# Kernel optimization log

Measured on AMD Instinct MI355X. Metric: run time of the kernel, lower is better.

## Reference

```python
import jax, jax.numpy as jnp
import numpy as np

IN_DIM, K, D, ITERS, EPS = 512, 8, 128, 3, 1e-8
LN_EPS = 1e-5

def _ln(x, g, b):
    m = jnp.mean(x, axis=-1, keepdims=True)
    v = jnp.var(x, axis=-1, keepdims=True)
    return (x - m) * jax.lax.rsqrt(v + LN_EPS) * g + b

def setup_inputs() -> dict:
    key = jax.random.key(0)
    ks = jax.random.split(key, 16)
    B, C, H, W = 64, IN_DIM, 32, 32
    s = lambda fan: 1.0 / np.sqrt(fan)
    inp = {
        'x': jax.random.normal(ks[0], (B, C, H, W), jnp.float32),
        'noise': jax.random.normal(ks[1], (B, K, D), jnp.float32),
        'slot_mu': jax.random.normal(ks[2], (1, K, D), jnp.float32) * 0.02,
        'slot_log_sigma': jnp.zeros((1, K, D), jnp.float32),
        'Wp': jax.random.uniform(ks[3], (IN_DIM, D), jnp.float32, -s(IN_DIM), s(IN_DIM)),
        'bp': jnp.zeros((D,), jnp.float32),
        'g_in': jnp.ones((D,), jnp.float32), 'b_in': jnp.zeros((D,), jnp.float32),
        'Wq': jax.random.uniform(ks[4], (D, D), jnp.float32, -s(D), s(D)),
        'bq': jnp.zeros((D,), jnp.float32),
        'Wk': jax.random.uniform(ks[5], (D, D), jnp.float32, -s(D), s(D)),
        'bk': jnp.zeros((D,), jnp.float32),
        'Wv': jax.random.uniform(ks[6], (D, D), jnp.float32, -s(D), s(D)),
        'bv': jnp.zeros((D,), jnp.float32),
        'W_ih': jax.random.uniform(ks[7], (3 * D, D), jnp.float32, -s(D), s(D)),
        'W_hh': jax.random.uniform(ks[8], (3 * D, D), jnp.float32, -s(D), s(D)),
        'b_ih': jax.random.uniform(ks[9], (3 * D,), jnp.float32, -s(D), s(D)),
        'b_hh': jax.random.uniform(ks[10], (3 * D,), jnp.float32, -s(D), s(D)),
        'W1': jax.random.uniform(ks[11], (D, 2 * D), jnp.float32, -s(D), s(D)),
        'b1': jnp.zeros((2 * D,), jnp.float32),
        'W2': jax.random.uniform(ks[12], (2 * D, D), jnp.float32, -s(2 * D), s(2 * D)),
        'b2': jnp.zeros((D,), jnp.float32),
        'g_slots': jnp.ones((D,), jnp.float32), 'b_slots': jnp.zeros((D,), jnp.float32),
        'g_mlp': jnp.ones((D,), jnp.float32), 'b_mlp': jnp.zeros((D,), jnp.float32),
    }
    return inp

def reference(x, noise, slot_mu, slot_log_sigma, Wp, bp, g_in, b_in,
              Wq, bq, Wk, bk, Wv, bv, W_ih, W_hh, b_ih, b_hh,
              W1, b1, W2, b2, g_slots, b_slots, g_mlp, b_mlp):
    B, C, H, W = x.shape
    N = H * W
    scale = D ** -0.5
    x_flat = x.reshape(B, C, N).transpose(0, 2, 1)          # [B,N,C]
    inputs = _ln(x_flat @ Wp + bp, g_in, b_in)              # [B,N,D]
    slots = slot_mu + jnp.exp(slot_log_sigma) * noise       # [B,K,D]
    k = inputs @ Wk + bk                                    # k/v are loop-invariant
    v = inputs @ Wv + bv
    attn = None
    for _ in range(ITERS):
        slots_prev = slots
        q = _ln(slots, g_slots, b_slots) @ Wq + bq          # [B,K,D]
        logits = jnp.einsum('bkd,bnd->bkn', q, k) * scale
        attn = jax.nn.softmax(logits, axis=1)               # softmax over slots
        attn_norm = attn / (jnp.sum(attn, axis=-1, keepdims=True) + EPS)
        updates = jnp.einsum('bkn,bnd->bkd', attn_norm, v)  # [B,K,D]
        # GRUCell (PyTorch gate order r,z,n)
        u2 = updates.reshape(B * K, D)
        h = slots_prev.reshape(B * K, D)
        gx = u2 @ W_ih.T + b_ih
        gh = h @ W_hh.T + b_hh
        xr, xz, xn = jnp.split(gx, 3, axis=-1)
        hr, hz, hn = jnp.split(gh, 3, axis=-1)
        r = jax.nn.sigmoid(xr + hr)
        z = jax.nn.sigmoid(xz + hz)
        n = jnp.tanh(xn + r * hn)
        slots = ((1.0 - z) * n + z * h).reshape(B, K, D)
        hmid = jax.nn.gelu(_ln(slots, g_mlp, b_mlp) @ W1 + b1, approximate=False)
        slots = slots + hmid @ W2 + b2
    return slots, attn
```

## Files before the change

### kernel.cpp

```cpp
#include <hip/hip_runtime.h>
#include <hip/hip_bf16.h>
#include <math.h>

#define B_ 64
#define C_ 512
#define N_ 1024
#define D_ 128
#define K_ 8

typedef __attribute__((ext_vector_type(8))) short bf16x8;
typedef __attribute__((ext_vector_type(4))) float f32x4;
typedef unsigned short ushort_t;

__device__ __forceinline__ unsigned short f2bs(float f) {
    union { __hip_bfloat16 h; unsigned short s; } u;
    u.h = __float2bfloat16(f);
    return u.s;
}
__device__ __forceinline__ float bs2f(unsigned short s) {
    union { unsigned int u; float f; } v;
    v.u = ((unsigned int)s) << 16;
    return v.f;
}
__device__ __forceinline__ float sigmoidf_(float x) { return 1.0f / (1.0f + expf(-x)); }
__device__ __forceinline__ float gelu_exact(float x) {
    return 0.5f * x * (1.0f + erff(x * 0.7071067811865476f));
}

__global__ __launch_bounds__(256) void prep_weights(
    const float* __restrict__ Wp, const float* __restrict__ Wk,
    const float* __restrict__ Wv, const float* __restrict__ W_ih,
    const float* __restrict__ W_hh,
    ushort_t* __restrict__ WpT, ushort_t* __restrict__ WkT,
    ushort_t* __restrict__ WvT, float* __restrict__ WTih,
    float* __restrict__ WThh)
{
    int tid = blockIdx.x * 256 + threadIdx.x;
    {
        int c = tid >> 7, d = tid & 127;
        WpT[d * 512 + c] = f2bs(Wp[tid]);
    }
    if (tid < 16384) {
        int c = tid >> 7, d = tid & 127;
        WkT[d * 128 + c] = f2bs(Wk[tid]);
        WvT[d * 128 + c] = f2bs(Wv[tid]);
    }
    if (tid < 49152) {
        int j = tid >> 7, c = tid & 127;
        WTih[c * 384 + j] = W_ih[tid];
        WThh[c * 384 + j] = W_hh[tid];
    }
}

__global__ __launch_bounds__(256) void proj_ln_mfma(
    const float* __restrict__ x, const ushort_t* __restrict__ WpT,
    const float* __restrict__ bp, const float* __restrict__ g_in,
    const float* __restrict__ b_in, ushort_t* __restrict__ outb)
{
    __shared__ ushort_t Al[64 * 40];
    __shared__ ushort_t Bl[128 * 40];
    __shared__ float red[64][2][2];
    const int t = threadIdx.x;
    const int b = blockIdx.x >> 4;
    const int n0 = (blockIdx.x & 15) << 6;
    const int w = t >> 6, lane = t & 63;
    const int quad = lane >> 4, m = lane & 15;
    const int rowoff = (w >> 1) << 5;
    const int coloff = (w & 1) << 6;

    f32x4 acc[2][4];
#pragma unroll
    for (int r = 0; r < 2; ++r)
#pragma unroll
        for (int c = 0; c < 4; ++c) acc[r][c] = (f32x4){0.f, 0.f, 0.f, 0.f};

    const float* xb = x + (size_t)b * (C_ * N_);
    for (int c0 = 0; c0 < C_; c0 += 32) {
#pragma unroll
        for (int i = 0; i < 8; ++i) {
            int idx = t + (i << 8);
            int cc = idx >> 6, nn = idx & 63;
            Al[nn * 40 + cc] = f2bs(xb[(size_t)(c0 + cc) * N_ + n0 + nn]);
        }
#pragma unroll
        for (int i = 0; i < 2; ++i) {
            int idx = t + (i << 8);
            int d = idx >> 2, seg = idx & 3;
            *(bf16x8*)&Bl[d * 40 + seg * 8] =
                *(const bf16x8*)&WpT[d * 512 + c0 + seg * 8];
        }
        __syncthreads();
        bf16x8 af[2], bfr[4];
#pragma unroll
        for (int r = 0; r < 2; ++r)
            af[r] = *(const bf16x8*)&Al[(rowoff + 16 * r + m) * 40 + quad * 8];
#pragma unroll
        for (int c = 0; c < 4; ++c)
            bfr[c] = *(const bf16x8*)&Bl[(coloff + 16 * c + m) * 40 + quad * 8];
#pragma unroll
        for (int r = 0; r < 2; ++r)
#pragma unroll
            for (int c = 0; c < 4; ++c)
                acc[r][c] = __builtin_amdgcn_mfma_f32_16x16x32_bf16(af[r], bfr[c], acc[r][c], 0, 0, 0);
        __syncthreads();
    }
    float gv[4], bv[4], bpv[4];
#pragma unroll
    for (int c = 0; c < 4; ++c) {
        int col = coloff + 16 * c + m;
        bpv[c] = bp[col]; gv[c] = g_in[col]; bv[c] = b_in[col];
    }
#pragma unroll
    for (int r = 0; r < 2; ++r)
#pragma unroll
        for (int c = 0; c < 4; ++c)
#pragma unroll
            for (int g = 0; g < 4; ++g) acc[r][c][g] += bpv[c];

#pragma unroll
    for (int r = 0; r < 2; ++r) {
#pragma unroll
        for (int g = 0; g < 4; ++g) {
            float s = 0.f, s2 = 0.f;
#pragma unroll
            for (int c = 0; c < 4; ++c) { float v = acc[r][c][g]; s += v; s2 += v * v; }
#pragma unroll
            for (int off = 1; off < 16; off <<= 1) {
                s += __shfl_xor(s, off, 64);
                s2 += __shfl_xor(s2, off, 64);
            }
            if (m == 0) {
                int row = rowoff + 16 * r + quad * 4 + g;
                red[row][w & 1][0] = s;
                red[row][w & 1][1] = s2;
            }
        }
    }
    __syncthreads();
#pragma unroll
    for (int r = 0; r < 2; ++r) {
#pragma unroll
        for (int g = 0; g < 4; ++g) {
            int row = rowoff + 16 * r + quad * 4 + g;
            float s = red[row][0][0] + red[row][1][0];
            float s2 = red[row][0][1] + red[row][1][1];
            float mean = s * (1.f / 128.f);
            float var = s2 * (1.f / 128.f) - mean * mean;
            float rs = rsqrtf(var + 1e-5f);
            size_t base = ((size_t)b * N_ + n0 + row) * D_;
#pragma unroll
            for (int c = 0; c < 4; ++c) {
                int col = coloff + 16 * c + m;
                float v = (acc[r][c][g] - mean) * rs * gv[c] + bv[c];
                outb[base + col] = f2bs(v);
            }
        }
    }
}

__global__ __launch_bounds__(256) void kv_mfma(
    const ushort_t* __restrict__ A,
    const ushort_t* __restrict__ WkT, const float* __restrict__ bk,
    const ushort_t* __restrict__ WvT, const float* __restrict__ bv,
    ushort_t* __restrict__ kout, ushort_t* __restrict__ vout)
{
    __shared__ ushort_t Al[64 * 40];
    __shared__ ushort_t Bk[128 * 40];
    __shared__ ushort_t Bv[128 * 40];
    const int t = threadIdx.x;
    const int row0 = blockIdx.x << 6;
    const int w = t >> 6, lane = t & 63;
    const int quad = lane >> 4, m = lane & 15;
    const int is_v = w >> 1;
    const int rowoff = (w & 1) << 5;

    f32x4 acc[2][8];
#pragma unroll
    for (int r = 0; r < 2; ++r)
#pragma unroll
        for (int c = 0; c < 8; ++c) acc[r][c] = (f32x4){0.f, 0.f, 0.f, 0.f};

    for (int c0 = 0; c0 < D_; c0 += 32) {
#pragma unroll
        for (int i = 0; i < 2; ++i) {
            int idx = t + (i << 8);
            int rr = idx >> 3, cc4 = (idx & 7) << 2;
            *(ushort4*)&Al[rr * 40 + cc4] =
                *(const ushort4*)&A[(size_t)(row0 + rr) * D_ + c0 + cc4];
        }
#pragma unroll
        for (int i = 0; i < 2; ++i) {
            int idx = t + (i << 8);
            int d = idx >> 2, seg = idx & 3;
            *(bf16x8*)&Bk[d * 40 + seg * 8] =
                *(const bf16x8*)&WkT[d * 128 + c0 + seg * 8];
            *(bf16x8*)&Bv[d * 40 + seg * 8] =
                *(const bf16x8*)&WvT[d * 128 + c0 + seg * 8];
        }
        __syncthreads();
        const ushort_t* Bsrc = is_v ? Bv : Bk;
        bf16x8 af[2], bfr[8];
#pragma unroll
        for (int r = 0; r < 2; ++r)
            af[r] = *(const bf16x8*)&Al[(rowoff + 16 * r + m) * 40 + quad * 8];
#pragma unroll
        for (int c = 0; c < 8; ++c)
            bfr[c] = *(const bf16x8*)&Bsrc[(16 * c + m) * 40 + quad * 8];
#pragma unroll
        for (int r = 0; r < 2; ++r)
#pragma unroll
            for (int c = 0; c < 8; ++c)
                acc[r][c] = __builtin_amdgcn_mfma_f32_16x16x32_bf16(af[r], bfr[c], acc[r][c], 0, 0, 0);
        __syncthreads();
    }
    const float* bias = is_v ? bv : bk;
    ushort_t* dst = is_v ? vout : kout;
    float bval[8];
#pragma unroll
    for (int c = 0; c < 8; ++c) bval[c] = bias[16 * c + m];
#pragma unroll
    for (int r = 0; r < 2; ++r) {
#pragma unroll
        for (int g = 0; g < 4; ++g) {
            int row = rowoff + 16 * r + quad * 4 + g;
            size_t base = (size_t)(row0 + row) * D_;
#pragma unroll
            for (int c = 0; c < 8; ++c)
                dst[base + 16 * c + m] = f2bs(acc[r][c][g] + bval[c]);
        }
    }
}

__global__ __launch_bounds__(256) void slots_init_kernel(
    const float* __restrict__ noise, const float* __restrict__ mu,
    const float* __restrict__ lsig, float* __restrict__ slots)
{
    int idx = blockIdx.x * 256 + threadIdx.x;
    int kd = idx & (K_ * D_ - 1);
    slots[idx] = mu[kd] + expf(lsig[kd]) * noise[idx];
}

__global__ __launch_bounds__(128) void q_ln_kernel(
    const float* __restrict__ slots, const float* __restrict__ g_slots,
    const float* __restrict__ b_slots, const float* __restrict__ Wq,
    const float* __restrict__ bq, float* __restrict__ qbuf,
    float* __restrict__ upd, float* __restrict__ S)
{
    __shared__ float sl[128], sl2[128];
    __shared__ float mrs[2];
    const int t = threadIdx.x;
    const int row = blockIdx.x;
    sl[t] = slots[(size_t)row * D_ + t];
    upd[(size_t)row * D_ + t] = 0.0f;
    if (t == 0) S[row] = 0.0f;
    __syncthreads();
    if (t < 64) {
        float v0 = sl[t], v1 = sl[t + 64];
        float s = v0 + v1, s2 = v0 * v0 + v1 * v1;
        for (int off = 32; off > 0; off >>= 1) {
            s += __shfl_down(s, off, 64);
            s2 += __shfl_down(s2, off, 64);
        }
        if (t == 0) {
            float mean = s * (1.f / 128.f);
            float var = s2 * (1.f / 128.f) - mean * mean;
            mrs[0] = mean; mrs[1] = rsqrtf(var + 1e-5f);
        }
    }
    __syncthreads();
    sl2[t] = (sl[t] - mrs[0]) * mrs[1] * g_slots[t] + b_slots[t];
    __syncthreads();
    float a = bq[t];
    for (int c = 0; c < 128; ++c) a = fmaf(sl2[c], Wq[(size_t)c * D_ + t], a);
    qbuf[(size_t)row * D_ + t] = a;
}

__global__ __launch_bounds__(256) void attn_kernel(
    const ushort_t* __restrict__ kb, const float* __restrict__ qbuf,
    float* __restrict__ attn, float* __restrict__ S,
    float* __restrict__ attn_out, int write_attn)
{
    __shared__ float qs[8][128];
    __shared__ float kt[64][129];
    __shared__ float lg[8][66];
    const int t = threadIdx.x;
    const int n0 = blockIdx.x << 6;
    const int b = blockIdx.y;
    const float SCALE = 0.08838834764831845f;

#pragma unroll
    for (int i = 0; i < 4; ++i) {
        int idx = t + (i << 8);
        int k = idx >> 7, d = idx & 127;
        qs[k][d] = qbuf[((size_t)b * K_ + k) * D_ + d];
    }
#pragma unroll
    for (int i = 0; i < 8; ++i) {
        int idx = t + (i << 8);
        int rr = idx >> 5, d4 = (idx & 31) << 2;
        ushort4 kv4 = *(const ushort4*)&kb[((size_t)b * N_ + n0 + rr) * D_ + d4];
        kt[rr][d4] = bs2f(kv4.x); kt[rr][d4 + 1] = bs2f(kv4.y);
        kt[rr][d4 + 2] = bs2f(kv4.z); kt[rr][d4 + 3] = bs2f(kv4.w);
    }
    __syncthreads();
    {
        int nn = t & 63, kg = t >> 6;
        float a0 = 0.f, a1 = 0.f;
        for (int d = 0; d < 128; ++d) {
            float kv = kt[nn][d];
            a0 = fmaf(qs[kg][d], kv, a0);
            a1 = fmaf(qs[kg + 4][d], kv, a1);
        }
        lg[kg][nn] = a0 * SCALE;
        lg[kg + 4][nn] = a1 * SCALE;
    }
    __syncthreads();
    if (t < 64) {
        float mx = lg[0][t];
#pragma unroll
        for (int k = 1; k < 8; ++k) mx = fmaxf(mx, lg[k][t]);
        float e[8]; float s = 0.f;
#pragma unroll
        for (int k = 0; k < 8; ++k) { e[k] = expf(lg[k][t] - mx); s += e[k]; }
        float inv = 1.0f / s;
#pragma unroll
        for (int k = 0; k < 8; ++k) lg[k][t] = e[k] * inv;
#pragma unroll
        for (int k = 0; k < 8; ++k) {
            float pv = e[k] * inv;
            for (int off = 32; off > 0; off >>= 1) pv += __shfl_down(pv, off, 64);
            if (t == 0) atomicAdd(&S[b * K_ + k], pv);
        }
    }
    __syncthreads();
    {
        int nn = t & 63, kg = t >> 6;
        float p0 = lg[kg][nn], p1 = lg[kg + 4][nn];
        size_t i0 = ((size_t)b * K_ + kg) * N_ + n0 + nn;
        size_t i1 = ((size_t)b * K_ + kg + 4) * N_ + n0 + nn;
        attn[i0] = p0;
        attn[i1] = p1;
        if (write_attn) { attn_out[i0] = p0; attn_out[i1] = p1; }
    }
}

__global__ __launch_bounds__(256) void updates_kernel(
    const float* __restrict__ attn, const ushort_t* __restrict__ vb,
    float* __restrict__ upd)
{
    __shared__ float vt[64][129];
    __shared__ float at[8][66];
    const int t = threadIdx.x;
    const int b = blockIdx.y;
    const int nbase = blockIdx.x << 8;
    const int d = t & 127, kk = t >> 7;
    float a0 = 0.f, a1 = 0.f, a2 = 0.f, a3 = 0.f;
    for (int st = 0; st < 4; ++st) {
        int n0 = nbase + (st << 6);
#pragma unroll
        for (int i = 0; i < 8; ++i) {
            int idx = t + (i << 8);
            int rr = idx >> 5, d4 = (idx & 31) << 2;
            ushort4 v4 = *(const ushort4*)&vb[((size_t)b * N_ + n0 + rr) * D_ + d4];
            vt[rr][d4] = bs2f(v4.x); vt[rr][d4 + 1] = bs2f(v4.y);
            vt[rr][d4 + 2] = bs2f(v4.z); vt[rr][d4 + 3] = bs2f(v4.w);
        }
#pragma unroll
        for (int i = 0; i < 2; ++i) {
            int idx = t + (i << 8);
            int k = idx >> 6, nn = idx & 63;
            at[k][nn] = attn[((size_t)b * K_ + k) * N_ + n0 + nn];
        }
        __syncthreads();
        for (int nn = 0; nn < 64; ++nn) {
            float vv = vt[nn][d];
            a0 = fmaf(at[kk][nn], vv, a0);
            a1 = fmaf(at[kk + 2][nn], vv, a1);
            a2 = fmaf(at[kk + 4][nn], vv, a2);
            a3 = fmaf(at[kk + 6][nn], vv, a3);
        }
        __syncthreads();
    }
    atomicAdd(&upd[((size_t)b * K_ + kk) * D_ + d], a0);
    atomicAdd(&upd[((size_t)b * K_ + kk + 2) * D_ + d], a1);
    atomicAdd(&upd[((size_t)b * K_ + kk + 4) * D_ + d], a2);
    atomicAdd(&upd[((size_t)b * K_ + kk + 6) * D_ + d], a3);
}

__global__ __launch_bounds__(256) void gru_mlp_kernel(
    const float* __restrict__ upd, const float* __restrict__ S,
    float* __restrict__ slots,
    const float* __restrict__ WTih, const float* __restrict__ WThh,
    const float* __restrict__ b_ih, const float* __restrict__ b_hh,
    const float* __restrict__ W1, const float* __restrict__ b1,
    const float* __restrict__ W2, const float* __restrict__ b2,
    const float* __restrict__ g_mlp, const float* __restrict__ b_mlp,
    float* __restrict__ out_slots, int final_iter)
{
    __shared__ float u[128], h[128], gx[384], gh[384], sn[128], tt[128], hm[256];
    __shared__ float mrs[2];
    const int t = threadIdx.x;
    const int row = blockIdx.x;
    if (t < 128) {
        float inv = 1.0f / (S[row] + 1e-8f);
        u[t] = upd[(size_t)row * D_ + t] * inv;
        h[t] = slots[(size_t)row * D_ + t];
    }
    __syncthreads();
    {
        int j = t;
        float ax = 0.f, ah = 0.f;
        for (int c = 0; c < 128; ++c) {
            float uc = u[c], hc = h[c];
            ax = fmaf(uc, WTih[(size_t)c * 384 + j], ax);
            ah = fmaf(hc, WThh[(size_t)c * 384 + j], ah);
        }
        gx[j] = ax + b_ih[j];
        gh[j] = ah + b_hh[j];
    }
    if (t < 128) {
        int j = 256 + t;
        float ax = 0.f, ah = 0.f;
        for (int c = 0; c < 128; ++c) {
            float uc = u[c], hc = h[c];
            ax = fmaf(uc, WTih[(size_t)c * 384 + j], ax);
            ah = fmaf(hc, WThh[(size_t)c * 384 + j], ah);
        }
        gx[j] = ax + b_ih[j];
        gh[j] = ah + b_hh[j];
    }
    __syncthreads();
    if (t < 128) {
        float r = sigmoidf_(gx[t] + gh[t]);
        float z = sigmoidf_(gx[t + 128] + gh[t + 128]);
        float nv = tanhf(gx[t + 256] + r * gh[t + 256]);
        sn[t] = (1.0f - z) * nv + z * h[t];
    }
    __syncthreads();
    if (t < 64) {
        float v0 = sn[t], v1 = sn[t + 64];
        float s = v0 + v1, s2 = v0 * v0 + v1 * v1;
        for (int off = 32; off > 0; off >>= 1) {
            s += __shfl_down(s, off, 64);
            s2 += __shfl_down(s2, off, 64);
        }
        if (t == 0) {
            float mean = s * (1.f / 128.f);
            float var = s2 * (1.f / 128.f) - mean * mean;
            mrs[0] = mean; mrs[1] = rsqrtf(var + 1e-5f);
        }
    }
    __syncthreads();
    if (t < 128) tt[t] = (sn[t] - mrs[0]) * mrs[1] * g_mlp[t] + b_mlp[t];
    __syncthreads();
    {
        float a = 0.f;
        for (int c = 0; c < 128; ++c) a = fmaf(tt[c], W1[(size_t)c * 256 + t], a);
        hm[t] = gelu_exact(a + b1[t]);
    }
    __syncthreads();
    if (t < 128) {
        float a = sn[t] + b2[t];
        for (int j = 0; j < 256; ++j) a = fmaf(hm[j], W2[(size_t)j * D_ + t], a);
        slots[(size_t)row * D_ + t] = a;
        if (final_iter) out_slots[(size_t)row * D_ + t] = a;
    }
}

extern "C" void kernel_launch(void* const* d_in, const int* in_sizes, int n_in,
                              void* d_out, int out_size, void* d_ws, size_t ws_size,
                              hipStream_t stream) {
    const float* x       = (const float*)d_in[0];
    const float* noise   = (const float*)d_in[1];
    const float* slot_mu = (const float*)d_in[2];
    const float* slot_ls = (const float*)d_in[3];
    const float* Wp      = (const float*)d_in[4];
    const float* bp      = (const float*)d_in[5];
    const float* g_in    = (const float*)d_in[6];
    const float* b_in    = (const float*)d_in[7];
    const float* Wq      = (const float*)d_in[8];
    const float* bq      = (const float*)d_in[9];
    const float* Wk      = (const float*)d_in[10];
    const float* bk      = (const float*)d_in[11];
    const float* Wv      = (const float*)d_in[12];
    const float* bv      = (const float*)d_in[13];
    const float* W_ih    = (const float*)d_in[14];
    const float* W_hh    = (const float*)d_in[15];
    const float* b_ih    = (const float*)d_in[16];
    const float* b_hh    = (const float*)d_in[17];
    const float* W1      = (const float*)d_in[18];
    const float* b1      = (const float*)d_in[19];
    const float* W2      = (const float*)d_in[20];
    const float* b2      = (const float*)d_in[21];
    const float* g_slots = (const float*)d_in[22];
    const float* b_slots = (const float*)d_in[23];
    const float* g_mlp   = (const float*)d_in[24];
    const float* b_mlp   = (const float*)d_in[25];

    float* out_slots = (float*)d_out;
    float* out_attn  = (float*)d_out + 65536;

    float* wsf = (float*)d_ws;
    ushort_t* inputsb = (ushort_t*)wsf;
    ushort_t* kb = (ushort_t*)(wsf + 4194304);
    ushort_t* vb = (ushort_t*)(wsf + 8388608);
    float* slots = wsf + 12582912;
    float* qbuf  = wsf + 12648448;
    float* attn  = wsf + 12713984;
    float* upd   = wsf + 13238272;
    float* S     = wsf + 13303808;
    ushort_t* WpT = (ushort_t*)(wsf + 13304320);
    ushort_t* WkT = (ushort_t*)(wsf + 13337088);
    ushort_t* WvT = (ushort_t*)(wsf + 13345280);
    float* WTih = wsf + 13353472;
    float* WThh = wsf + 13402624;

    prep_weights<<<dim3(256), dim3(256), 0, stream>>>(
        Wp, Wk, Wv, W_ih, W_hh, WpT, WkT, WvT, WTih, WThh);
    proj_ln_mfma<<<dim3(1024), dim3(256), 0, stream>>>(x, WpT, bp, g_in, b_in, inputsb);
    kv_mfma<<<dim3(1024), dim3(256), 0, stream>>>(inputsb, WkT, bk, WvT, bv, kb, vb);
    slots_init_kernel<<<dim3(256), dim3(256), 0, stream>>>(noise, slot_mu, slot_ls, slots);

    for (int it = 0; it < 3; ++it) {
        int last = (it == 2) ? 1 : 0;
        q_ln_kernel<<<dim3(512), dim3(128), 0, stream>>>(
            slots, g_slots, b_slots, Wq, bq, qbuf, upd, S);
        attn_kernel<<<dim3(16, 64), dim3(256), 0, stream>>>(
            kb, qbuf, attn, S, out_attn, last);
        updates_kernel<<<dim3(4, 64), dim3(256), 0, stream>>>(attn, vb, upd);
        gru_mlp_kernel<<<dim3(512), dim3(256), 0, stream>>>(
            upd, S, slots, WTih, WThh, b_ih, b_hh, W1, b1, W2, b2, g_mlp, b_mlp,
            out_slots, last);
    }
}
```

Before: 447.8 us.

## Fuse attention logits, softmax and PV into one kernel; fold q-proj into GRU

Merges the attention-logit/softmax kernel and the updates kernel into a single attn_pv kernel per (batch, quarter of N). The attention probabilities stay in shared memory instead of round-tripping through global memory, and per-block partial sums replace atomics. The slot LayerNorm plus Q projection moves into the tail of the GRU/MLP kernel, and slot init is fused with the first Q computation, cutting kernel launches per iteration from four to two. In exchange the fused kernel uses large shared memory with only 256 blocks of 512 threads, which may limit occupancy, and it adds a small reduction over the partial buffers.

Result: faster. 407.9 us (-8.9%).

```diff
diff --git a/kernel.cpp b/kernel.cpp
--- a/kernel.cpp
+++ b/kernel.cpp
@@ -231,28 +231,22 @@
     }
 }
 
-__global__ __launch_bounds__(256) void slots_init_kernel(
+__global__ __launch_bounds__(128) void init_q(
     const float* __restrict__ noise, const float* __restrict__ mu,
-    const float* __restrict__ lsig, float* __restrict__ slots)
-{
-    int idx = blockIdx.x * 256 + threadIdx.x;
-    int kd = idx & (K_ * D_ - 1);
-    slots[idx] = mu[kd] + expf(lsig[kd]) * noise[idx];
-}
-
-__global__ __launch_bounds__(128) void q_ln_kernel(
-    const float* __restrict__ slots, const float* __restrict__ g_slots,
-    const float* __restrict__ b_slots, const float* __restrict__ Wq,
-    const float* __restrict__ bq, float* __restrict__ qbuf,
-    float* __restrict__ upd, float* __restrict__ S)
+    const float* __restrict__ lsig,
+    const float* __restrict__ g_slots, const float* __restrict__ b_slots,
+    const float* __restrict__ Wq, const float* __restrict__ bq,
+    float* __restrict__ slots, float* __restrict__ qbuf)
 {
     __shared__ float sl[128], sl2[128];
     __shared__ float mrs[2];
     const int t = threadIdx.x;
     const int row = blockIdx.x;
-    sl[t] = slots[(size_t)row * D_ + t];
-    upd[(size_t)row * D_ + t] = 0.0f;
-    if (t == 0) S[row] = 0.0f;
+    const int b = row >> 3;
+    const int kd = (row & 7) * 128 + t;
+    float sv = mu[kd] + expf(lsig[kd]) * noise[b * 1024 + kd];
+    slots[(size_t)row * D_ + t] = sv;
+    sl[t] = sv;
     __syncthreads();
     if (t < 64) {
         float v0 = sl[t], v1 = sl[t + 64];
@@ -275,135 +269,183 @@
     qbuf[(size_t)row * D_ + t] = a;
 }
 
-__global__ __launch_bounds__(256) void attn_kernel(
-    const ushort_t* __restrict__ kb, const float* __restrict__ qbuf,
-    float* __restrict__ attn, float* __restrict__ S,
-    float* __restrict__ attn_out, int write_attn)
+__global__ __launch_bounds__(512, 2) void attn_pv(
+    const ushort_t* __restrict__ kb, const ushort_t* __restrict__ vb,
+    const float* __restrict__ qbuf,
+    float* __restrict__ S_part, float* __restrict__ upd_part,
+    float* __restrict__ out_attn, int last)
 {
-    __shared__ float qs[8][128];
-    __shared__ float kt[64][129];
-    __shared__ float lg[8][66];
+    __shared__ __align__(16) char scratch[69632];
+    __shared__ __align__(16) float at8[8][264];
+    __shared__ __align__(16) float qs[8][132];
+    __shared__ float red2[4][8];
+    ushort_t* kvt = (ushort_t*)scratch;
+    float* red = (float*)scratch;
+
     const int t = threadIdx.x;
-    const int n0 = blockIdx.x << 6;
-    const int b = blockIdx.y;
+    const int qd = blockIdx.x, b = blockIdx.y;
+    const int nbase = qd << 8;
+    const int wv = t >> 6, lane = t & 63;
     const float SCALE = 0.08838834764831845f;
 
-#pragma unroll
-    for (int i = 0; i < 4; ++i) {
-        int idx = t + (i << 8);
-        int k = idx >> 7, d = idx & 127;
-        qs[k][d] = qbuf[((size_t)b * K_ + k) * D_ + d];
-    }
+    for (int i = t; i < 1024; i += 512)
+        qs[i >> 7][i & 127] = qbuf[(size_t)b * 1024 + i];
 #pragma unroll
     for (int i = 0; i < 8; ++i) {
-        int idx = t + (i << 8);
-        int rr = idx >> 5, d4 = (idx & 31) << 2;
-        ushort4 kv4 = *(const ushort4*)&kb[((size_t)b * N_ + n0 + rr) * D_ + d4];
-        kt[rr][d4] = bs2f(kv4.x); kt[rr][d4 + 1] = bs2f(kv4.y);
-        kt[rr][d4 + 2] = bs2f(kv4.z); kt[rr][d4 + 3] = bs2f(kv4.w);
-    }
-    __syncthreads();
+        int idx = t + (i << 9);
+        int rr = idx >> 4, u8 = (idx & 15) << 3;
+        *(bf16x8*)&kvt[rr * 136 + u8] =
+            *(const bf16x8*)&kb[((size_t)b * N_ + nbase + rr) * D_ + u8];
+    }
+    __syncthreads();
+
     {
-        int nn = t & 63, kg = t >> 6;
-        float a0 = 0.f, a1 = 0.f;
-        for (int d = 0; d < 128; ++d) {
-            float kv = kt[nn][d];
-            a0 = fmaf(qs[kg][d], kv, a0);
-            a1 = fmaf(qs[kg + 4][d], kv, a1);
-        }
-        lg[kg][nn] = a0 * SCALE;
-        lg[kg + 4][nn] = a1 * SCALE;
-    }
-    __syncthreads();
-    if (t < 64) {
-        float mx = lg[0][t];
-#pragma unroll
-        for (int k = 1; k < 8; ++k) mx = fmaxf(mx, lg[k][t]);
-        float e[8]; float s = 0.f;
-#pragma unroll
-        for (int k = 0; k < 8; ++k) { e[k] = expf(lg[k][t] - mx); s += e[k]; }
-        float inv = 1.0f / s;
-#pragma unroll
-        for (int k = 0; k < 8; ++k) lg[k][t] = e[k] * inv;
+        const int rr = t & 255, kh = t >> 8;
+        float acc[4] = {0.f, 0.f, 0.f, 0.f};
+        for (int c0 = 0; c0 < 128; c0 += 8) {
+            bf16x8 kr = *(const bf16x8*)&kvt[rr * 136 + c0];
+            float kf[8];
+#pragma unroll
+            for (int j = 0; j < 8; ++j) kf[j] = bs2f((ushort_t)kr[j]);
+#pragma unroll
+            for (int kk = 0; kk < 4; ++kk) {
+                f32x4 qa = *(const f32x4*)&qs[4 * kh + kk][c0];
+                f32x4 qb = *(const f32x4*)&qs[4 * kh + kk][c0 + 4];
+                acc[kk] = fmaf(qa[0], kf[0], acc[kk]);
+                acc[kk] = fmaf(qa[1], kf[1], acc[kk]);
+                acc[kk] = fmaf(qa[2], kf[2], acc[kk]);
+                acc[kk] = fmaf(qa[3], kf[3], acc[kk]);
+                acc[kk] = fmaf(qb[0], kf[4], acc[kk]);
+                acc[kk] = fmaf(qb[1], kf[5], acc[kk]);
+                acc[kk] = fmaf(qb[2], kf[6], acc[kk]);
+                acc[kk] = fmaf(qb[3], kf[7], acc[kk]);
+            }
+        }
+#pragma unroll
+        for (int kk = 0; kk < 4; ++kk)
+            at8[4 * kh + kk][rr] = acc[kk];
+    }
+    __syncthreads();
+
+    if (t < 256) {
+        float l[8];
+#pragma unroll
+        for (int k = 0; k < 8; ++k) l[k] = at8[k][t] * SCALE;
+        float mx = l[0];
+#pragma unroll
+        for (int k = 1; k < 8; ++k) mx = fmaxf(mx, l[k]);
+        float e[8], ssum = 0.f;
+#pragma unroll
+        for (int k = 0; k < 8; ++k) { e[k] = expf(l[k] - mx); ssum += e[k]; }
+        float inv = 1.f / ssum;
+        float p[8];
 #pragma unroll
         for (int k = 0; k < 8; ++k) {
-            float pv = e[k] * inv;
-            for (int off = 32; off > 0; off >>= 1) pv += __shfl_down(pv, off, 64);
-            if (t == 0) atomicAdd(&S[b * K_ + k], pv);
-        }
-    }
-    __syncthreads();
+            p[k] = e[k] * inv;
+            at8[k][t] = p[k];
+            if (last) out_attn[((size_t)b * K_ + k) * N_ + nbase + t] = p[k];
+        }
+#pragma unroll
+        for (int k = 0; k < 8; ++k) {
+            float v = p[k];
+            for (int off = 32; off > 0; off >>= 1) v += __shfl_down(v, off, 64);
+            if (lane == 0) red2[wv][k] = v;
+        }
+    }
+    __syncthreads();
+    if (t < 8)
+        S_part[((size_t)b * 4 + qd) * 8 + t] =
+            red2[0][t] + red2[1][t] + red2[2][t] + red2[3][t];
+
+#pragma unroll
+    for (int i = 0; i < 8; ++i) {
+        int idx = t + (i << 9);
+        int rr = idx >> 4, u8 = (idx & 15) << 3;
+        *(bf16x8*)&kvt[rr * 136 + u8] =
+            *(const bf16x8*)&vb[((size_t)b * N_ + nbase + rr) * D_ + u8];
+    }
+    __syncthreads();
+
     {
-        int nn = t & 63, kg = t >> 6;
-        float p0 = lg[kg][nn], p1 = lg[kg + 4][nn];
-        size_t i0 = ((size_t)b * K_ + kg) * N_ + n0 + nn;
-        size_t i1 = ((size_t)b * K_ + kg + 4) * N_ + n0 + nn;
-        attn[i0] = p0;
-        attn[i1] = p1;
-        if (write_attn) { attn_out[i0] = p0; attn_out[i1] = p1; }
-    }
-}
-
-__global__ __launch_bounds__(256) void updates_kernel(
-    const float* __restrict__ attn, const ushort_t* __restrict__ vb,
-    float* __restrict__ upd)
-{
-    __shared__ float vt[64][129];
-    __shared__ float at[8][66];
-    const int t = threadIdx.x;
-    const int b = blockIdx.y;
-    const int nbase = blockIdx.x << 8;
-    const int d = t & 127, kk = t >> 7;
-    float a0 = 0.f, a1 = 0.f, a2 = 0.f, a3 = 0.f;
-    for (int st = 0; st < 4; ++st) {
-        int n0 = nbase + (st << 6);
-#pragma unroll
-        for (int i = 0; i < 8; ++i) {
-            int idx = t + (i << 8);
-            int rr = idx >> 5, d4 = (idx & 31) << 2;
-            ushort4 v4 = *(const ushort4*)&vb[((size_t)b * N_ + n0 + rr) * D_ + d4];
-            vt[rr][d4] = bs2f(v4.x); vt[rr][d4 + 1] = bs2f(v4.y);
-            vt[rr][d4 + 2] = bs2f(v4.z); vt[rr][d4 + 3] = bs2f(v4.w);
-        }
-#pragma unroll
-        for (int i = 0; i < 2; ++i) {
-            int idx = t + (i << 8);
-            int k = idx >> 6, nn = idx & 63;
-            at[k][nn] = attn[((size_t)b * K_ + k) * N_ + n0 + nn];
+        float acc[8][4];
+#pragma unroll
+        for (int k = 0; k < 8; ++k)
+#pragma unroll
+            for (int j = 0; j < 4; ++j) acc[k][j] = 0.f;
+        const int d4 = (t & 31) * 4, s = t >> 5;
+#pragma unroll
+        for (int i2 = 0; i2 < 4; ++i2) {
+            const int nn = (s << 4) + (i2 << 2);
+            float vf[4][4];
+#pragma unroll
+            for (int i = 0; i < 4; ++i) {
+                ushort4 v4 = *(const ushort4*)&kvt[(nn + i) * 136 + d4];
+                vf[i][0] = bs2f(v4.x); vf[i][1] = bs2f(v4.y);
+                vf[i][2] = bs2f(v4.z); vf[i][3] = bs2f(v4.w);
+            }
+#pragma unroll
+            for (int k = 0; k < 8; ++k) {
+                f32x4 a4 = *(const f32x4*)&at8[k][nn];
+#pragma unroll
+                for (int i = 0; i < 4; ++i) {
+                    acc[k][0] = fmaf(a4[i], vf[i][0], acc[k][0]);
+                    acc[k][1] = fmaf(a4[i], vf[i][1], acc[k][1]);
+                    acc[k][2] = fmaf(a4[i], vf[i][2], acc[k][2]);
+                    acc[k][3] = fmaf(a4[i], vf[i][3], acc[k][3]);
+                }
+            }
         }
         __syncthreads();
-        for (int nn = 0; nn < 64; ++nn) {
-            float vv = vt[nn][d];
-            a0 = fmaf(at[kk][nn], vv, a0);
-            a1 = fmaf(at[kk + 2][nn], vv, a1);
-            a2 = fmaf(at[kk + 4][nn], vv, a2);
-            a3 = fmaf(at[kk + 6][nn], vv, a3);
+#pragma unroll
+        for (int k = 0; k < 8; ++k)
+#pragma unroll
+            for (int j = 0; j < 4; ++j)
+                acc[k][j] += __shfl_xor(acc[k][j], 32, 64);
+        if (lane < 32) {
+#pragma unroll
+            for (int k = 0; k < 8; ++k)
+#pragma unroll
+                for (int j = 0; j < 4; ++j)
+                    red[(wv * 8 + k) * 132 + lane * 4 + j] = acc[k][j];
         }
         __syncthreads();
-    }
-    atomicAdd(&upd[((size_t)b * K_ + kk) * D_ + d], a0);
-    atomicAdd(&upd[((size_t)b * K_ + kk + 2) * D_ + d], a1);
-    atomicAdd(&upd[((size_t)b * K_ + kk + 4) * D_ + d], a2);
-    atomicAdd(&upd[((size_t)b * K_ + kk + 6) * D_ + d], a3);
-}
-
-__global__ __launch_bounds__(256) void gru_mlp_kernel(
-    const float* __restrict__ upd, const float* __restrict__ S,
+        for (int i = t; i < 1024; i += 512) {
+            int k = i >> 7, d = i & 127;
+            float ssum = 0.f;
+#pragma unroll
+            for (int w = 0; w < 8; ++w) ssum += red[(w * 8 + k) * 132 + d];
+            upd_part[((size_t)b * 4 + qd) * 1024 + i] = ssum;
+        }
+    }
+}
+
+__global__ __launch_bounds__(256) void gru_mlp_q(
+    const float* __restrict__ upd_part, const float* __restrict__ S_part,
     float* __restrict__ slots,
     const float* __restrict__ WTih, const float* __restrict__ WThh,
     const float* __restrict__ b_ih, const float* __restrict__ b_hh,
     const float* __restrict__ W1, const float* __restrict__ b1,
     const float* __restrict__ W2, const float* __restrict__ b2,
     const float* __restrict__ g_mlp, const float* __restrict__ b_mlp,
+    const float* __restrict__ g_slots, const float* __restrict__ b_slots,
+    const float* __restrict__ Wq, const float* __restrict__ bq,
+    float* __restrict__ qbuf,
     float* __restrict__ out_slots, int final_iter)
 {
     __shared__ float u[128], h[128], gx[384], gh[384], sn[128], tt[128], hm[256];
     __shared__ float mrs[2];
     const int t = threadIdx.x;
     const int row = blockIdx.x;
+    const int b = row >> 3, k = row & 7;
     if (t < 128) {
-        float inv = 1.0f / (S[row] + 1e-8f);
-        u[t] = upd[(size_t)row * D_ + t] * inv;
+        size_t sb = (size_t)b * 4;
+        float S = S_part[(sb + 0) * 8 + k] + S_part[(sb + 1) * 8 + k]
+                + S_part[(sb + 2) * 8 + k] + S_part[(sb + 3) * 8 + k];
+        float inv = 1.0f / (S + 1e-8f);
+        int i = k * 128 + t;
+        float up = upd_part[(sb + 0) * 1024 + i] + upd_part[(sb + 1) * 1024 + i]
+                 + upd_part[(sb + 2) * 1024 + i] + upd_part[(sb + 3) * 1024 + i];
+        u[t] = up * inv;
         h[t] = slots[(size_t)row * D_ + t];
     }
     __syncthreads();
@@ -464,6 +506,29 @@
         for (int j = 0; j < 256; ++j) a = fmaf(hm[j], W2[(size_t)j * D_ + t], a);
         slots[(size_t)row * D_ + t] = a;
         if (final_iter) out_slots[(size_t)row * D_ + t] = a;
+        u[t] = a;
+    }
+    __syncthreads();
+    if (t < 64) {
+        float v0 = u[t], v1 = u[t + 64];
+        float s = v0 + v1, s2 = v0 * v0 + v1 * v1;
+        for (int off = 32; off > 0; off >>= 1) {
+            s += __shfl_down(s, off, 64);
+            s2 += __shfl_down(s2, off, 64);
+        }
+        if (t == 0) {
+            float mean = s * (1.f / 128.f);
+            float var = s2 * (1.f / 128.f) - mean * mean;
+            mrs[0] = mean; mrs[1] = rsqrtf(var + 1e-5f);
+        }
+    }
+    __syncthreads();
+    if (t < 128) tt[t] = (u[t] - mrs[0]) * mrs[1] * g_slots[t] + b_slots[t];
+    __syncthreads();
+    if (!final_iter && t < 128) {
+        float a = bq[t];
+        for (int c = 0; c < 128; ++c) a = fmaf(tt[c], Wq[(size_t)c * D_ + t], a);
+        qbuf[(size_t)row * D_ + t] = a;
     }
 }
 
@@ -504,11 +569,10 @@
     ushort_t* inputsb = (ushort_t*)wsf;
     ushort_t* kb = (ushort_t*)(wsf + 4194304);
     ushort_t* vb = (ushort_t*)(wsf + 8388608);
-    float* slots = wsf + 12582912;
-    float* qbuf  = wsf + 12648448;
-    float* attn  = wsf + 12713984;
-    float* upd   = wsf + 13238272;
-    float* S     = wsf + 13303808;
+    float* slots    = wsf + 12582912;
+    float* qbuf     = wsf + 12648448;
+    float* upd_part = wsf + 12713984;
+    float* S_part   = wsf + 12976128;
     ushort_t* WpT = (ushort_t*)(wsf + 13304320);
     ushort_t* WkT = (ushort_t*)(wsf + 13337088);
     ushort_t* WvT = (ushort_t*)(wsf + 13345280);
@@ -519,17 +583,16 @@
         Wp, Wk, Wv, W_ih, W_hh, WpT, WkT, WvT, WTih, WThh);
     proj_ln_mfma<<<dim3(1024), dim3(256), 0, stream>>>(x, WpT, bp, g_in, b_in, inputsb);
     kv_mfma<<<dim3(1024), dim3(256), 0, stream>>>(inputsb, WkT, bk, WvT, bv, kb, vb);
-    slots_init_kernel<<<dim3(256), dim3(256), 0, stream>>>(noise, slot_mu, slot_ls, slots);
+    init_q<<<dim3(512), dim3(128), 0, stream>>>(
+        noise, slot_mu, slot_ls, g_slots, b_slots, Wq, bq, slots, qbuf);
 
     for (int it = 0; it < 3; ++it) {
         int last = (it == 2) ? 1 : 0;
-        q_ln_kernel<<<dim3(512), dim3(128), 0, stream>>>(
-            slots, g_slots, b_slots, Wq, bq, qbuf, upd, S);
-        attn_kernel<<<dim3(16, 64), dim3(256), 0, stream>>>(
-            kb, qbuf, attn, S, out_attn, last);
-        updates_kernel<<<dim3(4, 64), dim3(256), 0, stream>>>(attn, vb, upd);
-        gru_mlp_kernel<<<dim3(512), dim3(256), 0, stream>>>(
-            upd, S, slots, WTih, WThh, b_ih, b_hh, W1, b1, W2, b2, g_mlp, b_mlp,
-            out_slots, last);
-    }
-}
+        attn_pv<<<dim3(4, 64), dim3(512), 0, stream>>>(
+            kb, vb, qbuf, S_part, upd_part, out_attn, last);
+        gru_mlp_q<<<dim3(512), dim3(256), 0, stream>>>(
+            upd_part, S_part, slots, WTih, WThh, b_ih, b_hh,
+            W1, b1, W2, b2, g_mlp, b_mlp, g_slots, b_slots,
+            Wq, bq, qbuf, out_slots, last);
+    }
+}
```
